# Kernel optimization log

Measured on AMD Instinct MI355X. Metric: run time of the kernel, lower is better.

## Reference

```python
import jax, jax.numpy as jnp
import numpy as np

D_MODEL = 1024
NUM_HEADS = 16
D_K = D_MODEL // NUM_HEADS
B, S = 4, 2048


def setup_inputs() -> dict:
    key = jax.random.key(0)
    ks = jax.random.split(key, 11)
    s = 1.0 / np.sqrt(D_MODEL)  # torch Linear default init scale (uniform bound)
    def lin(k):
        kw, kb = jax.random.split(k)
        W = jax.random.uniform(kw, (D_MODEL, D_MODEL), jnp.float32, -s, s)
        b = jax.random.uniform(kb, (D_MODEL,), jnp.float32, -s, s)
        return W, b
    Wq, bq = lin(ks[0])
    Wk, bk = lin(ks[1])
    Wv, bv = lin(ks[2])
    Wo, bo = lin(ks[3])
    query = jax.random.normal(ks[4], (B, S, D_MODEL), jnp.float32)
    key_t = jax.random.normal(ks[5], (B, S, D_MODEL), jnp.float32)
    value = jax.random.normal(ks[6], (B, S, D_MODEL), jnp.float32)
    mask = jnp.ones((B, 1, 1, S), jnp.int32)
    return {"query": query, "key": key_t, "value": value, "mask": mask,
            "Wq": Wq, "bq": bq, "Wk": Wk, "bk": bk, "Wv": Wv, "bv": bv,
            "Wo": Wo, "bo": bo}


def _split_heads(x):
    # (B, S, D) -> (B, H, S, d_k)
    b, s, _ = x.shape
    return x.reshape(b, s, NUM_HEADS, D_K).transpose(0, 2, 1, 3)


def _mha(query, key, value, mask, Wq, bq, Wk, bk, Wv, bv, Wo, bo):
    Q = _split_heads(query @ Wq.T + bq)
    K = _split_heads(key @ Wk.T + bk)
    V = _split_heads(value @ Wv.T + bv)
    scores = jnp.einsum('bhqd,bhkd->bhqk', Q, K) / np.sqrt(D_K)
    scores = jnp.where(mask == 0, jnp.float32(-1e9), scores)
    attn = jax.nn.softmax(scores, axis=-1)
    out = jnp.einsum('bhqk,bhkd->bhqd', attn, V)  # (B,H,S,d_k)
    out = out.transpose(0, 2, 1, 3).reshape(out.shape[0], out.shape[2], D_MODEL)
    return out @ Wo.T + bo


def reference(query, key, value, mask, Wq, bq, Wk, bk, Wv, bv, Wo, bo):
    return _mha(query, key, value, mask, Wq, bq, Wk, bk, Wv, bv, Wo, bo)
```

## Files before the change

kernel.cpp:

```cpp
#include <hip/hip_runtime.h>


typedef unsigned short u16;
typedef __attribute__((ext_vector_type(8))) short short8;
typedef __attribute__((ext_vector_type(4))) float f32x4;

__device__ __forceinline__ u16 f2bf(float f) {
  union { float f; unsigned int u; } v; v.f = f;
  return (u16)((v.u + 0x7FFFu + ((v.u >> 16) & 1u)) >> 16);
}

__device__ __forceinline__ void gll16(const void* gptr, void* lptr) {
  __builtin_amdgcn_global_load_lds(
      (const __attribute__((address_space(1))) unsigned int*)gptr,
      (__attribute__((address_space(3))) unsigned int*)lptr, 16, 0, 0);
}

__global__ void cvt_x(const float* __restrict__ s, u16* __restrict__ d, int n) {
  const int i = (blockIdx.x * 256 + threadIdx.x) * 8;
  if (i >= n) return;
  f32x4 a = *(const f32x4*)(s + i);
  f32x4 b = *(const f32x4*)(s + i + 4);
  short8 r;
  r[0] = (short)f2bf(a[0]); r[1] = (short)f2bf(a[1]);
  r[2] = (short)f2bf(a[2]); r[3] = (short)f2bf(a[3]);
  r[4] = (short)f2bf(b[0]); r[5] = (short)f2bf(b[1]);
  r[6] = (short)f2bf(b[2]); r[7] = (short)f2bf(b[3]);
  *(short8*)(d + i) = r;
}

__global__ void cvt_w4(const float* __restrict__ w0, const float* __restrict__ w1,
                       const float* __restrict__ w2, const float* __restrict__ w3,
                       u16* __restrict__ d) {
  const int z = blockIdx.y;
  const float* s = (z == 0) ? w0 : (z == 1) ? w1 : (z == 2) ? w2 : w3;
  const int i = (blockIdx.x * 256 + threadIdx.x) * 8;
  u16* dz = d + (size_t)z * 1048576;
  f32x4 a = *(const f32x4*)(s + i);
  f32x4 b = *(const f32x4*)(s + i + 4);
  short8 r;
  r[0] = (short)f2bf(a[0]); r[1] = (short)f2bf(a[1]);
  r[2] = (short)f2bf(a[2]); r[3] = (short)f2bf(a[3]);
  r[4] = (short)f2bf(b[0]); r[5] = (short)f2bf(b[1]);
  r[6] = (short)f2bf(b[2]); r[7] = (short)f2bf(b[3]);
  *(short8*)(dz + i) = r;
}

#define GM 128
#define GN 128
#define GK 32

template <typename TC, bool TRANS>
__global__ __launch_bounds__(256, 3) void gemm_bb(
    const u16* __restrict__ A, const u16* __restrict__ W,
    const float* __restrict__ bias, TC* __restrict__ C,
    int M, int N, int K)
{
  __shared__ __align__(16) u16 As[2][GM * GK];
  __shared__ __align__(16) u16 Bs[2][GN * GK];

  const int tid  = threadIdx.x;
  const int lane = tid & 63;
  const int l15  = lane & 15;
  const int quad = lane >> 4;
  const int wave = tid >> 6;
  const int bm = blockIdx.y * GM;
  const int bn = blockIdx.x * GN;
  const int wm = (wave >> 1) * 64;
  const int wn = (wave & 1) * 64;

  const f32x4 zero4 = {0.f, 0.f, 0.f, 0.f};
  f32x4 acc[4][4];
#pragma unroll
  for (int i = 0; i < 4; i++)
#pragma unroll
    for (int j = 0; j < 4; j++) acc[i][j] = zero4;

  const int srow = tid >> 2;
  const int chl  = (tid & 3) ^ ((tid >> 3) & 3);
  const u16* Ag = A + (size_t)(bm + srow) * K + chl * 8;
  const u16* Wg = W + (size_t)(bn + srow) * K + chl * 8;
  const size_t rowskip = (size_t)64 * K;
  const int chpA = quad ^ ((l15 >> 1) & 3);

  gll16(Ag, &As[0][tid * 8]);
  gll16(Ag + rowskip, &As[0][tid * 8 + 2048]);
  gll16(Wg, &Bs[0][tid * 8]);
  gll16(Wg + rowskip, &Bs[0][tid * 8 + 2048]);

  int buf = 0;
  for (int k0 = 0; k0 < K; k0 += GK) {
    __syncthreads();
    if (k0 + GK < K) {
      const int nb = buf ^ 1;
      gll16(Ag + k0 + GK, &As[nb][tid * 8]);
      gll16(Ag + k0 + GK + rowskip, &As[nb][tid * 8 + 2048]);
      gll16(Wg + k0 + GK, &Bs[nb][tid * 8]);
      gll16(Wg + k0 + GK + rowskip, &Bs[nb][tid * 8 + 2048]);
    }

    short8 af[4], bfr[4];
#pragma unroll
    for (int mi = 0; mi < 4; mi++)
      af[mi] = *(const short8*)&As[buf][(wm + mi * 16 + l15) * GK + chpA * 8];
#pragma unroll
    for (int ni = 0; ni < 4; ni++)
      bfr[ni] = *(const short8*)&Bs[buf][(wn + ni * 16 + l15) * GK + chpA * 8];
#pragma unroll
    for (int mi = 0; mi < 4; mi++)
#pragma unroll
      for (int ni = 0; ni < 4; ni++)
        acc[mi][ni] = __builtin_amdgcn_mfma_f32_16x16x32_bf16(
            af[mi], bfr[ni], acc[mi][ni], 0, 0, 0);
    buf ^= 1;
  }

  float bval[4];
#pragma unroll
  for (int ni = 0; ni < 4; ni++) bval[ni] = bias[bn + wn + ni * 16 + l15];
#pragma unroll
  for (int mi = 0; mi < 4; mi++) {
    const int m0 = bm + wm + mi * 16 + quad * 4;
#pragma unroll
    for (int ni = 0; ni < 4; ni++) {
      const int n = bn + wn + ni * 16 + l15;
      if constexpr (TRANS) {
        ushort4 w;
        w.x = f2bf(acc[mi][ni][0] + bval[ni]);
        w.y = f2bf(acc[mi][ni][1] + bval[ni]);
        w.z = f2bf(acc[mi][ni][2] + bval[ni]);
        w.w = f2bf(acc[mi][ni][3] + bval[ni]);
        *(ushort4*)((u16*)C + (size_t)n * M + m0) = w;
      } else {
#pragma unroll
        for (int r = 0; r < 4; r++) {
          const float v = acc[mi][ni][r] + bval[ni];
          if constexpr (sizeof(TC) == 2)
            C[(size_t)(m0 + r) * N + n] = f2bf(v);
          else
            C[(size_t)(m0 + r) * N + n] = v;
        }
      }
    }
  }
}

__global__ __launch_bounds__(256, 3) void attn_fused(
    const u16* __restrict__ Qb, const u16* __restrict__ Kb,
    const u16* __restrict__ VtG, const int* __restrict__ mask,
    u16* __restrict__ Ob)
{
  constexpr int S = 2048, D = 1024;
  __shared__ __align__(16) u16 Ks[2][64 * 64];
  __shared__ __align__(16) u16 Vs[2][64 * 64];
  __shared__ __align__(16) u16 Pt[4][32 * 64];

  const int tid  = threadIdx.x;
  const int lane = tid & 63;
  const int wave = tid >> 6;
  const int l15  = lane & 15;
  const int quad = lane >> 4;
  const int b = blockIdx.y >> 4;
  const int h = blockIdx.y & 15;
  const int qw = blockIdx.x * 128 + wave * 32;

  const u16* Qp = Qb + (size_t)b * S * D + h * 64;
  const u16* Kp = Kb + (size_t)b * S * D + h * 64;
  const u16* Vg = VtG + (size_t)h * 64 * 8192 + b * 2048;
  const int* mp = mask + b * S;

  short8 qf[2][2];
#pragma unroll
  for (int qb = 0; qb < 2; qb++)
#pragma unroll
    for (int c = 0; c < 2; c++)
      qf[qb][c] = *(const short8*)&Qp[(size_t)(qw + qb * 16 + l15) * D + c * 32 + quad * 8];

  const f32x4 zero4 = {0.f, 0.f, 0.f, 0.f};
  f32x4 o_acc[2][4];
#pragma unroll
  for (int qb = 0; qb < 2; qb++)
#pragma unroll
    for (int ni = 0; ni < 4; ni++) o_acc[qb][ni] = zero4;
  float rsum[2] = {0.f, 0.f};

  const int srow = tid >> 3;
  const int chl  = (tid & 7) ^ (srow & 7);
  const int fsw  = l15 & 7;

#pragma unroll
  for (int p = 0; p < 2; p++) {
    gll16(Kp + (size_t)(p * 32 + srow) * D + chl * 8, &Ks[0][p * 2048 + tid * 8]);
    gll16(Vg + (size_t)(p * 32 + srow) * 8192 + chl * 8, &Vs[0][p * 2048 + tid * 8]);
  }

  f32x4 cm[4];
#pragma unroll
  for (int s = 0; s < 4; s++) {
    int4 mv = *(const int4*)&mp[s * 16 + quad * 4];
    cm[s][0] = mv.x ? 0.f : -1.0e9f;
    cm[s][1] = mv.y ? 0.f : -1.0e9f;
    cm[s][2] = mv.z ? 0.f : -1.0e9f;
    cm[s][3] = mv.w ? 0.f : -1.0e9f;
  }

  constexpr float SCL2 = 0.125f * 1.44269504f;

  int buf = 0;
  for (int kt = 0; kt < S; kt += 64) {
    __syncthreads();

    if (kt + 64 < S) {
      const int nb = buf ^ 1;
#pragma unroll
      for (int p = 0; p < 2; p++) {
        gll16(Kp + (size_t)(kt + 64 + p * 32 + srow) * D + chl * 8,
              &Ks[nb][p * 2048 + tid * 8]);
        gll16(Vg + (size_t)(p * 32 + srow) * 8192 + kt + 64 + chl * 8,
              &Vs[nb][p * 2048 + tid * 8]);
      }
    }
    f32x4 nm[4];
    const int nkt = (kt + 64) & (S - 1);
#pragma unroll
    for (int s = 0; s < 4; s++) {
      int4 mv = *(const int4*)&mp[nkt + s * 16 + quad * 4];
      nm[s][0] = mv.x ? 0.f : -1.0e9f;
      nm[s][1] = mv.y ? 0.f : -1.0e9f;
      nm[s][2] = mv.z ? 0.f : -1.0e9f;
      nm[s][3] = mv.w ? 0.f : -1.0e9f;
    }

    f32x4 sc[2][4];
#pragma unroll
    for (int qb = 0; qb < 2; qb++)
#pragma unroll
      for (int s = 0; s < 4; s++) sc[qb][s] = zero4;
#pragma unroll
    for (int c = 0; c < 2; c++)
#pragma unroll
      for (int s = 0; s < 4; s++) {
        short8 kf = *(const short8*)
            &Ks[buf][(s * 16 + l15) * 64 + ((c * 4 + quad) ^ fsw) * 8];
        sc[0][s] = __builtin_amdgcn_mfma_f32_16x16x32_bf16(kf, qf[0][c], sc[0][s], 0, 0, 0);
        sc[1][s] = __builtin_amdgcn_mfma_f32_16x16x32_bf16(kf, qf[1][c], sc[1][s], 0, 0, 0);
      }

#pragma unroll
    for (int qb = 0; qb < 2; qb++) {
      const int qrow = qb * 16 + l15;
#pragma unroll
      for (int s = 0; s < 4; s++) {
        unsigned int t[4];
#pragma unroll
        for (int r = 0; r < 4; r++) {
          const float sv = fmaf(sc[qb][s][r], SCL2, cm[s][r]);
          const float p = __builtin_amdgcn_exp2f(sv);
          union { float f; unsigned int u; } pu; pu.f = p;
          t[r] = pu.u & 0xffff0000u;
          union { unsigned int u; float f; } tf; tf.u = t[r];
          rsum[qb] += tf.f;
        }
        uint2 w;
        w.x = t[1] | (t[0] >> 16);
        w.y = t[3] | (t[2] >> 16);
        const int phys = (s * 2 + (quad >> 1)) ^ fsw;
        *(uint2*)&Pt[wave][qrow * 64 + phys * 8 + (quad & 1) * 4] = w;
      }
    }

#pragma unroll
    for (int c = 0; c < 2; c++) {
      short8 pf[2];
#pragma unroll
      for (int qb = 0; qb < 2; qb++)
        pf[qb] = *(const short8*)
            &Pt[wave][(qb * 16 + l15) * 64 + ((c * 4 + quad) ^ fsw) * 8];
#pragma unroll
      for (int ni = 0; ni < 4; ni++) {
        short8 vf = *(const short8*)
            &Vs[buf][(ni * 16 + l15) * 64 + ((c * 4 + quad) ^ fsw) * 8];
        o_acc[0][ni] = __builtin_amdgcn_mfma_f32_16x16x32_bf16(pf[0], vf, o_acc[0][ni], 0, 0, 0);
        o_acc[1][ni] = __builtin_amdgcn_mfma_f32_16x16x32_bf16(pf[1], vf, o_acc[1][ni], 0, 0, 0);
      }
    }

#pragma unroll
    for (int s = 0; s < 4; s++) cm[s] = nm[s];
    buf ^= 1;
  }

  float rl[2][4];
#pragma unroll
  for (int qb = 0; qb < 2; qb++) {
    float x = rsum[qb];
    x += __shfl_xor(x, 16, 64);
    x += __shfl_xor(x, 32, 64);
#pragma unroll
    for (int r = 0; r < 4; r++)
      rl[qb][r] = 1.0f / __shfl(x, quad * 4 + r, 64);
  }
#pragma unroll
  for (int qb = 0; qb < 2; qb++) {
    const int q0 = qw + qb * 16 + quad * 4;
#pragma unroll
    for (int ni = 0; ni < 4; ni++)
#pragma unroll
      for (int r = 0; r < 4; r++)
        Ob[(size_t)(b * S + q0 + r) * D + h * 64 + ni * 16 + l15] =
            f2bf(o_acc[qb][ni][r] * rl[qb][r]);
  }
}

extern "C" void kernel_launch(void* const* d_in, const int* in_sizes, int n_in,
                              void* d_out, int out_size, void* d_ws, size_t ws_size,
                              hipStream_t stream) {
  const int M = 8192, N = 1024, K = 1024;
  const float* q    = (const float*)d_in[0];
  const float* k    = (const float*)d_in[1];
  const float* v    = (const float*)d_in[2];
  const int*   mask = (const int*)d_in[3];
  const float* Wq = (const float*)d_in[4];
  const float* bq = (const float*)d_in[5];
  const float* Wk = (const float*)d_in[6];
  const float* bk = (const float*)d_in[7];
  const float* Wv = (const float*)d_in[8];
  const float* bv = (const float*)d_in[9];
  const float* Wo = (const float*)d_in[10];
  const float* bo = (const float*)d_in[11];

  const size_t MN = (size_t)M * N;
  u16* Qb  = (u16*)d_ws;
  u16* Kb  = Qb + MN;
  u16* VtG = Kb + MN;
  u16* Ob  = VtG + MN;
  u16* Wc  = Ob + MN;

  dim3 bb(256);
  dim3 gg(N / GN, M / GM);
  const int xblk = M * N / (256 * 8);

  cvt_w4<<<dim3(512, 4), bb, 0, stream>>>(Wq, Wk, Wv, Wo, Wc);

  cvt_x<<<xblk, bb, 0, stream>>>(q, Ob, M * N);
  gemm_bb<u16, false><<<gg, bb, 0, stream>>>(Ob, Wc + 0 * 1048576, bq, Qb, M, N, K);
  cvt_x<<<xblk, bb, 0, stream>>>(k, Ob, M * N);
  gemm_bb<u16, false><<<gg, bb, 0, stream>>>(Ob, Wc + 1 * 1048576, bk, Kb, M, N, K);
  cvt_x<<<xblk, bb, 0, stream>>>(v, Ob, M * N);
  gemm_bb<u16, true><<<gg, bb, 0, stream>>>(Ob, Wc + 2 * 1048576, bv, VtG, M, N, K);

  attn_fused<<<dim3(16, 64), bb, 0, stream>>>(Qb, Kb, VtG, mask, Ob);

  gemm_bb<float, false><<<gg, bb, 0, stream>>>(Ob, Wc + 3 * 1048576, bo, (float*)d_out, M, N, K);
}
```

Before: 393.6 us.

## Enlarge GEMM tile to 256x128 with 512 threads and merge conversion kernels

The projection GEMMs move from 128x128 tiles with 4 waves to 256x128 tiles with 8 waves. Each weight tile loaded into LDS now feeds twice as many rows, and the grid halves to 256 blocks. All float-to-bf16 conversions (q, k, v and the four weights) are fused into one launch writing separate buffers, with the workspace aliased so later stages reuse dead buffers. This removes three kernel launches and the serial convert/GEMM alternation. The cost is one block per CU with reduced wave-level occupancy, plus a coupling to the unseen epilogue's indexing.

```diff
diff --git a/kernel.cpp b/kernel.cpp
--- a/kernel.cpp
+++ b/kernel.cpp
@@ -16,42 +16,45 @@
       (__attribute__((address_space(3))) unsigned int*)lptr, 16, 0, 0);
 }
 
-__global__ void cvt_x(const float* __restrict__ s, u16* __restrict__ d, int n) {
-  const int i = (blockIdx.x * 256 + threadIdx.x) * 8;
-  if (i >= n) return;
-  f32x4 a = *(const f32x4*)(s + i);
-  f32x4 b = *(const f32x4*)(s + i + 4);
+__global__ void cvt_all(const float* __restrict__ q, const float* __restrict__ k,
+                        const float* __restrict__ v,
+                        const float* __restrict__ w0, const float* __restrict__ w1,
+                        const float* __restrict__ w2, const float* __restrict__ w3,
+                        u16* __restrict__ Xq, u16* __restrict__ Xk,
+                        u16* __restrict__ Xv, u16* __restrict__ Wc)
+{
+  const int z = blockIdx.y;
+  const long long i = ((long long)blockIdx.x * 256 + threadIdx.x) * 8;
+  const float* s;
+  u16* d;
+  long long so;
+  if (z < 3) {
+    s = (z == 0) ? q : (z == 1) ? k : v;
+    d = ((z == 0) ? Xq : (z == 1) ? Xk : Xv) + i;
+    so = i;
+  } else {
+    if (i >= 4194304) return;
+    const int w = (int)(i >> 20);
+    s = (w == 0) ? w0 : (w == 1) ? w1 : (w == 2) ? w2 : w3;
+    so = i & 1048575;
+    d = Wc + i;
+  }
+  f32x4 a = *(const f32x4*)(s + so);
+  f32x4 b = *(const f32x4*)(s + so + 4);
   short8 r;
   r[0] = (short)f2bf(a[0]); r[1] = (short)f2bf(a[1]);
   r[2] = (short)f2bf(a[2]); r[3] = (short)f2bf(a[3]);
   r[4] = (short)f2bf(b[0]); r[5] = (short)f2bf(b[1]);
   r[6] = (short)f2bf(b[2]); r[7] = (short)f2bf(b[3]);
-  *(short8*)(d + i) = r;
-}
-
-__global__ void cvt_w4(const float* __restrict__ w0, const float* __restrict__ w1,
-                       const float* __restrict__ w2, const float* __restrict__ w3,
-                       u16* __restrict__ d) {
-  const int z = blockIdx.y;
-  const float* s = (z == 0) ? w0 : (z == 1) ? w1 : (z == 2) ? w2 : w3;
-  const int i = (blockIdx.x * 256 + threadIdx.x) * 8;
-  u16* dz = d + (size_t)z * 1048576;
-  f32x4 a = *(const f32x4*)(s + i);
-  f32x4 b = *(const f32x4*)(s + i + 4);
-  short8 r;
-  r[0] = (short)f2bf(a[0]); r[1] = (short)f2bf(a[1]);
-  r[2] = (short)f2bf(a[2]); r[3] = (short)f2bf(a[3]);
-  r[4] = (short)f2bf(b[0]); r[5] = (short)f2bf(b[1]);
-  r[6] = (short)f2bf(b[2]); r[7] = (short)f2bf(b[3]);
-  *(short8*)(dz + i) = r;
-}
-
-#define GM 128
+  *(short8*)d = r;
+}
+
+#define GM 256
 #define GN 128
 #define GK 32
 
 template <typename TC, bool TRANS>
-__global__ __launch_bounds__(256, 3) void gemm_bb(
+__global__ __launch_bounds__(512, 2) void gemm_bb(
     const u16* __restrict__ A, const u16* __restrict__ W,
     const float* __restrict__ bias, TC* __restrict__ C,
     int M, int N, int K)
@@ -66,8 +69,8 @@
   const int wave = tid >> 6;
   const int bm = blockIdx.y * GM;
   const int bn = blockIdx.x * GN;
-  const int wm = (wave >> 1) * 64;
-  const int wn = (wave & 1) * 64;
+  const int wm = (wave & 3) * 64;
+  const int wn = (wave >> 2) * 64;
 
   const f32x4 zero4 = {0.f, 0.f, 0.f, 0.f};
   f32x4 acc[4][4];
@@ -80,13 +83,12 @@
   const int chl  = (tid & 3) ^ ((tid >> 3) & 3);
   const u16* Ag = A + (size_t)(bm + srow) * K + chl * 8;
   const u16* Wg = W + (size_t)(bn + srow) * K + chl * 8;
-  const size_t rowskip = (size_t)64 * K;
+  const size_t rowskipA = (size_t)128 * K;
   const int chpA = quad ^ ((l15 >> 1) & 3);
 
   gll16(Ag, &As[0][tid * 8]);
-  gll16(Ag + rowskip, &As[0][tid * 8 + 2048]);
+  gll16(Ag + rowskipA, &As[0][tid * 8 + 4096]);
   gll16(Wg, &Bs[0][tid * 8]);
-  gll16(Wg + rowskip, &Bs[0][tid * 8 + 2048]);
 
   int buf = 0;
   for (int k0 = 0; k0 < K; k0 += GK) {
@@ -94,9 +96,8 @@
     if (k0 + GK < K) {
       const int nb = buf ^ 1;
       gll16(Ag + k0 + GK, &As[nb][tid * 8]);
-      gll16(Ag + k0 + GK + rowskip, &As[nb][tid * 8 + 2048]);
+      gll16(Ag + k0 + GK + rowskipA, &As[nb][tid * 8 + 4096]);
       gll16(Wg + k0 + GK, &Bs[nb][tid * 8]);
-      gll16(Wg + k0 + GK + rowskip, &Bs[nb][tid * 8 + 2048]);
     }
 
     short8 af[4], bfr[4];
@@ -330,26 +331,26 @@
   const float* bo = (const float*)d_in[11];
 
   const size_t MN = (size_t)M * N;
-  u16* Qb  = (u16*)d_ws;
-  u16* Kb  = Qb + MN;
-  u16* VtG = Kb + MN;
-  u16* Ob  = VtG + MN;
-  u16* Wc  = Ob + MN;
+  u16* Xq = (u16*)d_ws;
+  u16* Xk = Xq + MN;
+  u16* Xv = Xk + MN;
+  u16* Qb = Xv + MN;
+  u16* Wc = Qb + MN;
+  u16* Kb  = Xq;
+  u16* VtG = Xk;
+  u16* Ob  = Xv;
 
   dim3 bb(256);
   dim3 gg(N / GN, M / GM);
-  const int xblk = M * N / (256 * 8);
-
-  cvt_w4<<<dim3(512, 4), bb, 0, stream>>>(Wq, Wk, Wv, Wo, Wc);
-
-  cvt_x<<<xblk, bb, 0, stream>>>(q, Ob, M * N);
-  gemm_bb<u16, false><<<gg, bb, 0, stream>>>(Ob, Wc + 0 * 1048576, bq, Qb, M, N, K);
-  cvt_x<<<xblk, bb, 0, stream>>>(k, Ob, M * N);
-  gemm_bb<u16, false><<<gg, bb, 0, stream>>>(Ob, Wc + 1 * 1048576, bk, Kb, M, N, K);
-  cvt_x<<<xblk, bb, 0, stream>>>(v, Ob, M * N);
-  gemm_bb<u16, true><<<gg, bb, 0, stream>>>(Ob, Wc + 2 * 1048576, bv, VtG, M, N, K);
+
+  cvt_all<<<dim3(4096, 4), bb, 0, stream>>>(q, k, v, Wq, Wk, Wv, Wo,
+                                            Xq, Xk, Xv, Wc);
+
+  gemm_bb<u16, false><<<gg, dim3(512), 0, stream>>>(Xq, Wc + 0 * 1048576, bq, Qb, M, N, K);
+  gemm_bb<u16, false><<<gg, dim3(512), 0, stream>>>(Xk, Wc + 1 * 1048576, bk, Kb, M, N, K);
+  gemm_bb<u16, true ><<<gg, dim3(512), 0, stream>>>(Xv, Wc + 2 * 1048576, bv, VtG, M, N, K);
 
   attn_fused<<<dim3(16, 64), bb, 0, stream>>>(Qb, Kb, VtG, mask, Ob);
 
-  gemm_bb<float, false><<<gg, bb, 0, stream>>>(Ob, Wc + 3 * 1048576, bo, (float*)d_out, M, N, K);
-}
+  gemm_bb<float, false><<<gg, dim3(512), 0, stream>>>(Ob, Wc + 3 * 1048576, bo, (float*)d_out, M, N, K);
+}
```

Result: slower. 404.0 us (+2.6%).
